# Kernel optimization log

Hardware: AMD Instinct MI355X
Metric: run time of the kernel (lower is better)

Reference implementation:

```python
import jax, jax.numpy as jnp
import numpy as np

B, T = 512, 64
STOCH, DETER, HIDDEN = 30, 200, 200
A, EMBED = 12, 1024
MIN_STD = 0.1
UPDATE_BIAS = -1.0


def _linear_init(key, fan_in, fan_out):
    w_key, b_key = jax.random.split(key)
    lim = 1.0 / np.sqrt(fan_in)
    W = jax.random.uniform(w_key, (fan_in, fan_out), minval=-lim, maxval=lim, dtype=jnp.float32)
    b = jax.random.uniform(b_key, (fan_out,), minval=-lim, maxval=lim, dtype=jnp.float32)
    return W, b


def setup_inputs() -> dict:
    key = jax.random.key(0)
    ks = jax.random.split(key, 12)
    embed = jax.random.normal(ks[0], (B, T, EMBED), dtype=jnp.float32)
    action = jax.random.normal(ks[1], (B, T, A), dtype=jnp.float32)
    noise_prior = jax.random.normal(ks[2], (B, T, STOCH), dtype=jnp.float32)
    noise_post = jax.random.normal(ks[3], (B, T, STOCH), dtype=jnp.float32)
    inp_W, inp_b = _linear_init(ks[4], STOCH + A, HIDDEN)          # _inp_layers
    gru_W, gru_b = _linear_init(ks[5], HIDDEN + DETER, 3 * DETER)  # GRUCell._layer
    img_out_W, img_out_b = _linear_init(ks[6], DETER, HIDDEN)      # _img_out_layers
    ims_W, ims_b = _linear_init(ks[7], HIDDEN, 2 * STOCH)          # _ims_stat_layer
    obs_out_W, obs_out_b = _linear_init(ks[8], DETER + EMBED, HIDDEN)  # _obs_out_layers
    obs_W, obs_b = _linear_init(ks[9], HIDDEN, 2 * STOCH)          # _obs_stat_layer
    return dict(embed=embed, action=action, noise_prior=noise_prior, noise_post=noise_post,
                inp_W=inp_W, inp_b=inp_b, gru_W=gru_W, gru_b=gru_b,
                img_out_W=img_out_W, img_out_b=img_out_b, ims_W=ims_W, ims_b=ims_b,
                obs_out_W=obs_out_W, obs_out_b=obs_out_b, obs_W=obs_W, obs_b=obs_b)


def _observe(embed, action, noise_prior, noise_post,
             inp_W, inp_b, gru_W, gru_b, img_out_W, img_out_b,
             ims_W, ims_b, obs_out_W, obs_out_b, obs_W, obs_b):
    # time-major for scan: [T, B, ...]
    emb_t = jnp.swapaxes(embed, 0, 1)
    act_t = jnp.swapaxes(action, 0, 1)
    npr_t = jnp.swapaxes(noise_prior, 0, 1)
    npo_t = jnp.swapaxes(noise_post, 0, 1)

    def step(carry, xs):
        stoch, deter = carry                    # posterior stoch [B,STOCH], deter [B,DETER]
        a, e, nz_pr, nz_po = xs
        # img_step: input MLP
        x = jax.nn.elu(jnp.concatenate([stoch, a], -1) @ inp_W + inp_b)
        # GRUCell (norm=False)
        parts = jnp.concatenate([x, deter], -1) @ gru_W + gru_b   # [B, 3*DETER]
        reset, cand, update = jnp.split(parts, 3, -1)
        reset = jax.nn.sigmoid(reset)
        cand = jnp.tanh(reset * cand)
        update = jax.nn.sigmoid(update + UPDATE_BIAS)
        deter_new = update * cand + (1.0 - update) * deter
        # prior stats
        h = jax.nn.elu(deter_new @ img_out_W + img_out_b)
        mean_pr, std_pr = jnp.split(h @ ims_W + ims_b, 2, -1)
        std_pr = jax.nn.softplus(std_pr) + MIN_STD
        stoch_pr = mean_pr + std_pr * nz_pr
        # posterior (temp_post=True): cat(deter, embed)
        ho = jax.nn.elu(jnp.concatenate([deter_new, e], -1) @ obs_out_W + obs_out_b)
        mean_po, std_po = jnp.split(ho @ obs_W + obs_b, 2, -1)
        std_po = jax.nn.softplus(std_po) + MIN_STD
        stoch_po = mean_po + std_po * nz_po
        out = (stoch_po, mean_po, std_po, stoch_pr, mean_pr, std_pr, deter_new)
        return (stoch_po, deter_new), out

    init = (jnp.zeros((B, STOCH), jnp.float32), jnp.zeros((B, DETER), jnp.float32))
    _, outs = jax.lax.scan(step, init, (act_t, emb_t, npr_t, npo_t))
    # back to batch-major and pack into a single array [B, T, 6*STOCH + DETER]
    outs = [jnp.swapaxes(o, 0, 1) for o in outs]
    return jnp.concatenate(outs, -1)


def reference(embed, action, noise_prior, noise_post,
              inp_W, inp_b, gru_W, gru_b, img_out_W, img_out_b,
              ims_W, ims_b, obs_out_W, obs_out_b, obs_W, obs_b):
    return _observe(embed, action, noise_prior, noise_post,
                    inp_W, inp_b, gru_W, gru_b, img_out_W, img_out_b,
                    ims_W, ims_b, obs_out_W, obs_out_b, obs_W, obs_b)
```

## Files before the change

### kernel.cpp

```cpp
#include <hip/hip_runtime.h>

typedef _Float16 h2   __attribute__((ext_vector_type(2)));
typedef _Float16 h4   __attribute__((ext_vector_type(4)));
typedef _Float16 half8 __attribute__((ext_vector_type(8)));
typedef float f32x4   __attribute__((ext_vector_type(4)));

#define MFMA16(a,b,c) __builtin_amdgcn_mfma_f32_16x16x32_f16((a),(b),(c),0,0,0)
#define ATOMIC_ST(p,v) __hip_atomic_store((p),(v),__ATOMIC_RELAXED,__HIP_MEMORY_SCOPE_AGENT)
#define ATOMIC_LD(p)   __hip_atomic_load((p),__ATOMIC_RELAXED,__HIP_MEMORY_SCOPE_AGENT)
#define BAR_LDS() do { asm volatile("s_waitcnt lgkmcnt(0)" ::: "memory"); \
                       __builtin_amdgcn_s_barrier();                      \
                       asm volatile("" ::: "memory"); } while (0)


#define EP_HALVES ((size_t)32768*208)

__global__ void prep_frags(const float* __restrict__ inpW, const float* __restrict__ gruW,
                           const float* __restrict__ imgW, const float* __restrict__ obsoutW,
                           const float* __restrict__ imsW, const float* __restrict__ obsW,
                           _Float16* __restrict__ frags) {
    int gb = blockIdx.x, lane = threadIdx.x;
    const float* src; int KS, K, N, ld, roff = 0, local;
    if (gb < 26)       { src = inpW;    KS = 2;  K = 42;   N = 200; ld = 200; local = gb; }
    else if (gb < 520) { src = gruW;    KS = 13; K = 400;  N = 600; ld = 600; local = gb - 26; }
    else if (gb < 611) { src = imgW;    KS = 7;  K = 200;  N = 200; ld = 200; local = gb - 520; }
    else if (gb < 702) { src = obsoutW; KS = 7;  K = 200;  N = 200; ld = 200; local = gb - 611; }
    else if (gb < 730) { src = imsW;    KS = 7;  K = 200;  N = 60;  ld = 60;  local = gb - 702; }
    else if (gb < 758) { src = obsW;    KS = 7;  K = 200;  N = 60;  ld = 60;  local = gb - 730; }
    else               { src = obsoutW; KS = 32; K = 1024; N = 200; ld = 200; roff = 200; local = gb - 758; }
    int nt = local / KS, ks = local % KS;
    int n  = nt * 16 + (lane & 15);
    int k0 = ks * 32 + (lane >> 4) * 8;
    half8 v;
#pragma unroll
    for (int j = 0; j < 8; ++j) {
        int k = k0 + j;
        float f = (k < K && n < N) ? src[(size_t)(k + roff) * ld + n] : 0.0f;
        v[j] = (_Float16)f;
    }
    *(half8*)(frags + (size_t)gb * 512 + lane * 8) = v;
}

__global__ __launch_bounds__(256) void ep_gemm(const float* __restrict__ embed,
                                               const _Float16* __restrict__ w2f,
                                               _Float16* __restrict__ ep) {
    __shared__ __align__(16) _Float16 aE[16 * 1048];
    int tid = threadIdx.x;
    int rb = blockIdx.x * 16;
#pragma unroll
    for (int i = 0; i < 16; ++i) {
        float4 e = *((const float4*)(embed + (size_t)(rb + i) * 1024) + tid);
        h4 hv; hv[0] = (_Float16)e.x; hv[1] = (_Float16)e.y; hv[2] = (_Float16)e.z; hv[3] = (_Float16)e.w;
        *(h4*)(aE + i * 1048 + tid * 4) = hv;
    }
    __syncthreads();
    int w = tid >> 6, lane = tid & 63, m = lane & 15, q = lane >> 4;
    f32x4 acc[4] = {};
    int nts[4]; int ntc = 0;
    for (int nt = w; nt < 13; nt += 4) nts[ntc++] = nt;
    half8 bb[2][4];
#pragma unroll
    for (int j = 0; j < 4; ++j) if (j < ntc)
        bb[0][j] = *(const half8*)(w2f + ((size_t)(nts[j] * 32) * 64 + lane) * 8);
#pragma unroll
    for (int ks = 0; ks < 32; ++ks) {
        int cur = ks & 1, nxt = cur ^ 1;
        if (ks < 31) {
#pragma unroll
            for (int j = 0; j < 4; ++j) if (j < ntc)
                bb[nxt][j] = *(const half8*)(w2f + ((size_t)(nts[j] * 32 + ks + 1) * 64 + lane) * 8);
        }
        half8 a = *(const half8*)(aE + m * 1048 + ks * 32 + q * 8);
#pragma unroll
        for (int j = 0; j < 4; ++j) if (j < ntc)
            acc[j] = MFMA16(a, bb[cur][j], acc[j]);
    }
    for (int j = 0; j < ntc; ++j) {
        int col = nts[j] * 16 + m;
#pragma unroll
        for (int i = 0; i < 4; ++i)
            ep[(size_t)(rb + q * 4 + i) * 208 + col] = (_Float16)acc[j][i];
    }
}

__device__ __forceinline__ float sigm_(float x) { return 1.0f / (1.0f + __expf(-x)); }
__device__ __forceinline__ float tanh_(float x) { float e = __expf(2.0f * x); return 1.0f - 2.0f / (e + 1.0f); }
__device__ __forceinline__ float elu_(float x)  { return x > 0.0f ? x : __expf(x) - 1.0f; }
__device__ __forceinline__ float sp_(float x)   { return fmaxf(x, 0.0f) + log1pf(__expf(-fabsf(x))); }
__device__ __forceinline__ unsigned packh2(float a, float b) {
    h2 p; p[0] = (_Float16)a; p[1] = (_Float16)b;
    return __builtin_bit_cast(unsigned, p);
}

__global__ __launch_bounds__(512) __attribute__((amdgpu_waves_per_eu(2, 2))) void rssm_scan(
    const float* __restrict__ action, const float* __restrict__ npr, const float* __restrict__ npo,
    const float* __restrict__ inp_b, const float* __restrict__ gru_b,
    const float* __restrict__ img_b, const float* __restrict__ obsout_b,
    const float* __restrict__ ims_b, const float* __restrict__ obs_b,
    const _Float16* __restrict__ frags, const _Float16* __restrict__ ep,
    unsigned* __restrict__ qdet, unsigned* __restrict__ stochb,
    unsigned* __restrict__ flags, float* __restrict__ out) {

    __shared__ __align__(16) unsigned actI[16 * 36];
    __shared__ __align__(16) unsigned actG[16 * 212];
    __shared__ __align__(16) unsigned actX[16 * 116];
    __shared__ __align__(16) _Float16 parts[16 * 208];
    __shared__ float statspre[16 * 65];
    __shared__ float bias[1320];

    const _Float16* Finp  = frags;
    const _Float16* Fgru  = frags + (size_t)26  * 512;
    const _Float16* Fimg  = frags + (size_t)520 * 512;
    const _Float16* Fobsd = frags + (size_t)611 * 512;
    const _Float16* Fims  = frags + (size_t)702 * 512;
    const _Float16* Fobs  = frags + (size_t)730 * 512;

    const int tid = threadIdx.x, w = tid >> 6, lane = tid & 63, m = lane & 15, q = lane >> 4;
    const int g = blockIdx.x & 31, wg = blockIdx.x >> 5;
    const int rb = g * 16;
    const bool post = (wg >= 2);
    const bool statside = (wg == 0) || (wg == 2);
    const int colA = w * 16 + m;
    const int colB = (8 + w) * 16 + m;
    unsigned* gf = flags + g * 512;

    for (int i = tid; i < 1320; i += 512) {
        float v;
        if (i < 200) v = inp_b[i];
        else if (i < 800)  v = gru_b[i - 200];
        else if (i < 1000) v = img_b[i - 800];
        else if (i < 1200) v = obsout_b[i - 1000];
        else if (i < 1260) v = ims_b[i - 1200];
        else               v = obs_b[i - 1260];
        bias[i] = v;
    }
    for (int i = tid; i < 16 * 36;  i += 512) actI[i] = 0u;
    for (int i = tid; i < 16 * 212; i += 512) actG[i] = 0u;
    for (int i = tid; i < 16 * 116; i += 512) actX[i] = 0u;

    half8 bgru0[13];
    {
        int tA = (w < 4) ? (3 * wg + w) : (12 + 3 * wg + (w - 4));
#pragma unroll
        for (int ks = 0; ks < 13; ++ks)
            bgru0[ks] = *(const half8*)(Fgru + ((size_t)(tA * 13 + ks) * 64 + lane) * 8);
    }
    half8 bgru1[13];
    if (w < 4) {
        int tB = 25 + 3 * wg + w;
#pragma unroll
        for (int ks = 0; ks < 13; ++ks)
            bgru1[ks] = *(const half8*)(Fgru + ((size_t)(tB * 13 + ks) * 64 + lane) * 8);
    }
    half8 bi0[2], bi1[2];
#pragma unroll
    for (int ks = 0; ks < 2; ++ks)
        bi0[ks] = *(const half8*)(Finp + ((size_t)(w * 2 + ks) * 64 + lane) * 8);
    if (w < 5) {
#pragma unroll
        for (int ks = 0; ks < 2; ++ks)
            bi1[ks] = *(const half8*)(Finp + ((size_t)((8 + w) * 2 + ks) * 64 + lane) * 8);
    }
    const _Float16* F3 = post ? Fobsd : Fimg;
    const _Float16* F4 = post ? Fobs : Fims;
    half8 bp3a[7];
    if (statside) {
#pragma unroll
        for (int ks = 0; ks < 7; ++ks)
            bp3a[ks] = *(const half8*)(F3 + ((size_t)(w * 7 + ks) * 64 + lane) * 8);
    }
    half8 bp4[7];
    if (statside && w >= 4) {
#pragma unroll
        for (int ks = 0; ks < 7; ++ks)
            bp4[ks] = *(const half8*)(F4 + ((size_t)((w - 4) * 7 + ks) * 64 + lane) * 8);
    }
    __syncthreads();

    for (int t = 0; t < 64; ++t) {
        h2 epA[4], epB[4];
        if (post && !(m & 1)) {
#pragma unroll
            for (int i = 0; i < 4; ++i)
                epA[i] = *(const h2*)(ep + ((size_t)(rb + q * 4 + i) * 64 + t) * 208 + colA);
            if (w < 5 && colB < 200) {
#pragma unroll
                for (int i = 0; i < 4; ++i)
                    epB[i] = *(const h2*)(ep + ((size_t)(rb + q * 4 + i) * 64 + t) * 208 + colB);
            }
        }

        if (t > 0 && wg != 2) {
            if (tid == 0) {
                unsigned* f = gf + (t - 1) * 8 + 4;
                int it = 0;
                while (ATOMIC_LD(f) != (unsigned)t) {
                    __builtin_amdgcn_s_sleep(1);
                    if (++it > (1 << 20)) break;
                }
            }
            BAR_LDS();
            __atomic_signal_fence(__ATOMIC_ACQUIRE);
            if (tid < 240) {
                int r = tid / 15, cp = tid % 15;
                actI[r * 36 + cp] =
                    ATOMIC_LD(stochb + (size_t)((((t - 1) & 1) * 32 + g)) * 256 + r * 16 + cp);
            }
        }
        if (tid < 96) {
            int r = tid / 6, cp = tid % 6;
            float2 a2 = *(const float2*)(action + ((size_t)(rb + r) * 64 + t) * 12 + 2 * cp);
            actI[r * 36 + 15 + cp] = packh2(a2.x, a2.y);
        }
        float2 nz = make_float2(0.0f, 0.0f);
        if (statside && tid < 240) {
            int r = tid / 15, cp = tid % 15;
            const float* ns = post ? npo : npr;
            nz = *(const float2*)(ns + ((size_t)(rb + r) * 64 + t) * 30 + 2 * cp);
        }
        BAR_LDS();

        {
            f32x4 acc = {}, acc2 = {};
#pragma unroll
            for (int ks = 0; ks < 2; ++ks) {
                half8 a = *(const half8*)(actI + m * 36 + ks * 16 + q * 4);
                acc = MFMA16(a, bi0[ks], acc);
                if (w < 5) acc2 = MFMA16(a, bi1[ks], acc2);
            }
            f32x4 accN;
#pragma unroll
            for (int i = 0; i < 4; ++i) accN[i] = __shfl_xor(acc[i], 1);
            if (!(m & 1)) {
                int col = w * 16 + m;
#pragma unroll
                for (int i = 0; i < 4; ++i)
                    actG[(q * 4 + i) * 212 + (col >> 1)] =
                        packh2(elu_(acc[i] + bias[col]), elu_(accN[i] + bias[col + 1]));
            }
            if (w < 5) {
                f32x4 acc2N;
#pragma unroll
                for (int i = 0; i < 4; ++i) acc2N[i] = __shfl_xor(acc2[i], 1);
                if (!(m & 1)) {
                    int col = (8 + w) * 16 + m;
                    if (col < 200) {
#pragma unroll
                        for (int i = 0; i < 4; ++i)
                            actG[(q * 4 + i) * 212 + (col >> 1)] =
                                packh2(elu_(acc2[i] + bias[col]), elu_(acc2N[i] + bias[col + 1]));
                    }
                }
            }
        }
        BAR_LDS();

        {
            f32x4 a0 = {}, a1 = {};
#pragma unroll
            for (int ks = 0; ks < 13; ++ks) {
                half8 a = *(const half8*)(actG + m * 212 + ks * 16 + q * 4);
                a0 = MFMA16(a, bgru0[ks], a0);
                if (w < 4) a1 = MFMA16(a, bgru1[ks], a1);
            }
#pragma unroll
            for (int i = 0; i < 4; ++i)
                parts[(q * 4 + i) * 208 + w * 16 + m] = (_Float16)a0[i];
            if (w < 4) {
#pragma unroll
                for (int i = 0; i < 4; ++i)
                    parts[(q * 4 + i) * 208 + (8 + w) * 16 + m] = (_Float16)a1[i];
            }
        }
        half8 pf3[7];
        if (statside && w < 5) {
#pragma unroll
            for (int ks = 0; ks < 7; ++ks)
                pf3[ks] = *(const half8*)(F3 + ((size_t)((8 + w) * 7 + ks) * 64 + lane) * 8);
        }
        BAR_LDS();

        unsigned* qd = qdet + (size_t)((t & 1) * 32 + g) * 1600;
        float gdn0 = 0.0f, gdn1 = 0.0f; int gr = 0, gn0 = 0;
        if (tid < 400) {
            int r = tid / 25, p = tid % 25;
            int n0 = 50 * wg + 2 * p;
            float pg[3][2];
#pragma unroll
            for (int j = 0; j < 3; ++j) {
                int cg = n0 + 200 * j;
                int bj = (j == 0) ? 3 * wg : (j == 1) ? 12 + 3 * wg : 25 + 3 * wg;
                int lt = 4 * j + (cg >> 4) - bj;
                h2 v = *(const h2*)(parts + r * 208 + lt * 16 + (cg & 15));
                pg[j][0] = (float)v[0] + bias[200 + cg];
                pg[j][1] = (float)v[1] + bias[200 + cg + 1];
            }
            h2 dold = *(const h2*)&actG[r * 212 + 100 + (n0 >> 1)];
            float dn[2];
#pragma unroll
            for (int e = 0; e < 2; ++e) {
                float reset = sigm_(pg[0][e]);
                float cand  = tanh_(reset * pg[1][e]);
                float upd   = sigm_(pg[2][e] - 1.0f);
                dn[e] = upd * cand + (1.0f - upd) * (float)dold[e];
            }
            unsigned pk = packh2(dn[0], dn[1]);
            actG[r * 212 + 100 + (n0 >> 1)] = pk;
            ATOMIC_ST(qd + r * 100 + (n0 >> 1), pk);
            gdn0 = dn[0]; gdn1 = dn[1]; gr = r; gn0 = n0;
        }
        __syncthreads();

        __atomic_signal_fence(__ATOMIC_RELEASE);
        if (tid == 0) ATOMIC_ST(gf + t * 8 + wg, (unsigned)(t + 1));
        if (tid < 400)
            *(float2*)(out + ((size_t)(rb + gr) * 64 + t) * 380 + 180 + gn0) = make_float2(gdn0, gdn1);
        if (tid < 3) {
            unsigned* f = gf + t * 8 + ((wg + 1 + tid) & 3);
            int it = 0;
            while (ATOMIC_LD(f) != (unsigned)(t + 1)) {
                __builtin_amdgcn_s_sleep(1);
                if (++it > (1 << 20)) break;
            }
        }
        BAR_LDS();
        __atomic_signal_fence(__ATOMIC_ACQUIRE);
        for (int i = tid; i < 1200; i += 512) {
            int r = i / 75, idx = i % 75;
            int pp = (25 * (wg + 1) + idx) % 100;
            actG[r * 212 + 100 + pp] = ATOMIC_LD(qd + r * 100 + pp);
        }
        BAR_LDS();

        if (statside) {
            f32x4 acc = {}, acc2 = {};
#pragma unroll
            for (int ks = 0; ks < 7; ++ks) {
                half8 a = *(const half8*)(actG + m * 212 + 100 + ks * 16 + q * 4);
                acc = MFMA16(a, bp3a[ks], acc);
                if (w < 5) acc2 = MFMA16(a, pf3[ks], acc2);
            }
            f32x4 accN;
#pragma unroll
            for (int i = 0; i < 4; ++i) accN[i] = __shfl_xor(acc[i], 1);
            if (!(m & 1)) {
                int bb0 = post ? 1000 : 800;
#pragma unroll
                for (int i = 0; i < 4; ++i) {
                    float e0 = post ? (float)epA[i][0] : 0.0f;
                    float e1 = post ? (float)epA[i][1] : 0.0f;
                    actX[(q * 4 + i) * 116 + (colA >> 1)] =
                        packh2(elu_(acc[i] + bias[bb0 + colA] + e0),
                               elu_(accN[i] + bias[bb0 + colA + 1] + e1));
                }
            }
            if (w < 5) {
                f32x4 acc2N;
#pragma unroll
                for (int i = 0; i < 4; ++i) acc2N[i] = __shfl_xor(acc2[i], 1);
                if (!(m & 1) && colB < 200) {
                    int bb0 = post ? 1000 : 800;
#pragma unroll
                    for (int i = 0; i < 4; ++i) {
                        float e0 = post ? (float)epB[i][0] : 0.0f;
                        float e1 = post ? (float)epB[i][1] : 0.0f;
                        actX[(q * 4 + i) * 116 + (colB >> 1)] =
                            packh2(elu_(acc2[i] + bias[bb0 + colB] + e0),
                                   elu_(acc2N[i] + bias[bb0 + colB + 1] + e1));
                    }
                }
            }
        }
        BAR_LDS();

        if (statside && w >= 4) {
            f32x4 acc = {};
#pragma unroll
            for (int ks = 0; ks < 7; ++ks) {
                half8 a = *(const half8*)(actX + m * 116 + ks * 16 + q * 4);
                acc = MFMA16(a, bp4[ks], acc);
            }
#pragma unroll
            for (int i = 0; i < 4; ++i)
                statspre[(q * 4 + i) * 65 + (w - 4) * 16 + m] = acc[i];
        }
        BAR_LDS();

        float o0v = 0.f, o1v = 0.f, o2v = 0.f, o3v = 0.f, o4v = 0.f, o5v = 0.f;
        int pr = 0, pcp = 0; bool doout = false;
        if (statside && tid < 240) {
            int r = tid / 15, cp = tid % 15;
            int bb0 = post ? 1260 : 1200;
            float m0 = statspre[r * 65 + 2 * cp]     + bias[bb0 + 2 * cp];
            float m1 = statspre[r * 65 + 2 * cp + 1] + bias[bb0 + 2 * cp + 1];
            float s0 = sp_(statspre[r * 65 + 30 + 2 * cp]     + bias[bb0 + 30 + 2 * cp]) + 0.1f;
            float s1 = sp_(statspre[r * 65 + 30 + 2 * cp + 1] + bias[bb0 + 30 + 2 * cp + 1]) + 0.1f;
            float st0 = m0 + s0 * nz.x, st1 = m1 + s1 * nz.y;
            if (post) {
                unsigned pk = packh2(st0, st1);
                actI[r * 36 + cp] = pk;
                ATOMIC_ST(stochb + (size_t)((t & 1) * 32 + g) * 256 + r * 16 + cp, pk);
            }
            o0v = st0; o1v = st1; o2v = m0; o3v = m1; o4v = s0; o5v = s1;
            pr = r; pcp = cp; doout = true;
        }
        __syncthreads();
        if (wg == 2 && t < 63) {
            __atomic_signal_fence(__ATOMIC_RELEASE);
            if (tid == 0) ATOMIC_ST(gf + t * 8 + 4, (unsigned)(t + 1));
        }
        if (doout) {
            size_t ob = ((size_t)(rb + pr) * 64 + t) * 380;
            int o0 = post ? 0 : 90;
            *(float2*)(out + ob + o0 + 2 * pcp)      = make_float2(o0v, o1v);
            *(float2*)(out + ob + o0 + 30 + 2 * pcp) = make_float2(o2v, o3v);
            *(float2*)(out + ob + o0 + 60 + 2 * pcp) = make_float2(o4v, o5v);
        }
    }
}

extern "C" void kernel_launch(void* const* d_in, const int* in_sizes, int n_in,
                              void* d_out, int out_size, void* d_ws, size_t ws_size,
                              hipStream_t stream) {
    const float* embed   = (const float*)d_in[0];
    const float* action  = (const float*)d_in[1];
    const float* npr     = (const float*)d_in[2];
    const float* npo     = (const float*)d_in[3];
    const float* inpW    = (const float*)d_in[4];
    const float* inpb    = (const float*)d_in[5];
    const float* gruW    = (const float*)d_in[6];
    const float* grub    = (const float*)d_in[7];
    const float* imgW    = (const float*)d_in[8];
    const float* imgb    = (const float*)d_in[9];
    const float* imsW    = (const float*)d_in[10];
    const float* imsb    = (const float*)d_in[11];
    const float* obsoutW = (const float*)d_in[12];
    const float* obsoutb = (const float*)d_in[13];
    const float* obsW    = (const float*)d_in[14];
    const float* obsb    = (const float*)d_in[15];

    char* ws = (char*)d_ws;
    _Float16* ep     = (_Float16*)ws;
    _Float16* frags  = (_Float16*)(ws + EP_HALVES * 2);
    char* p          = ws + EP_HALVES * 2 + (size_t)1174 * 1024;
    unsigned* qdetb  = (unsigned*)p;
    p += (size_t)2 * 32 * 1600 * 4;
    unsigned* stochb = (unsigned*)p;
    p += (size_t)2 * 32 * 256 * 4;
    unsigned* flags  = (unsigned*)p;

    prep_frags<<<1174, 64, 0, stream>>>(inpW, gruW, imgW, obsoutW, imsW, obsW, frags);
    ep_gemm<<<2048, 256, 0, stream>>>(embed, frags + (size_t)758 * 512, ep);
    rssm_scan<<<128, 512, 0, stream>>>(action, npr, npo, inpb, grub, imgb, obsoutb,
                                       imsb, obsb, frags, ep, qdetb, stochb, flags,
                                       (float*)d_out);
}
```

Measured before the change: 948.8 us.

## Replace flag-based cross-block sync with tagged 64-bit data words polled per element

Cross-workgroup exchange of the deter and stoch state now packs a step tag into the upper half of each 64-bit word. Consumers poll each word until its tag matches, which removes the separate flag stores, the flag polling and several block-wide barriers on each timestep. The ep intermediate is also stored with a row stride of 200 instead of 208, and ep_gemm zeroes the exchange buffers so stale tags from earlier runs cannot match. The cost is wider atomics, more polling traffic from many threads, and a reliance on ordering between each 64-bit store and its payload.

```diff
diff --git a/kernel.cpp b/kernel.cpp
--- a/kernel.cpp
+++ b/kernel.cpp
@@ -4,16 +4,18 @@
 typedef _Float16 h4   __attribute__((ext_vector_type(4)));
 typedef _Float16 half8 __attribute__((ext_vector_type(8)));
 typedef float f32x4   __attribute__((ext_vector_type(4)));
+typedef unsigned long long u64;
 
 #define MFMA16(a,b,c) __builtin_amdgcn_mfma_f32_16x16x32_f16((a),(b),(c),0,0,0)
-#define ATOMIC_ST(p,v) __hip_atomic_store((p),(v),__ATOMIC_RELAXED,__HIP_MEMORY_SCOPE_AGENT)
-#define ATOMIC_LD(p)   __hip_atomic_load((p),__ATOMIC_RELAXED,__HIP_MEMORY_SCOPE_AGENT)
+#define ATOMIC_ST64(p,v) __hip_atomic_store((p),(v),__ATOMIC_RELAXED,__HIP_MEMORY_SCOPE_AGENT)
+#define ATOMIC_LD64(p)   __hip_atomic_load((p),__ATOMIC_RELAXED,__HIP_MEMORY_SCOPE_AGENT)
 #define BAR_LDS() do { asm volatile("s_waitcnt lgkmcnt(0)" ::: "memory"); \
                        __builtin_amdgcn_s_barrier();                      \
                        asm volatile("" ::: "memory"); } while (0)
 
 
-#define EP_HALVES ((size_t)32768*208)
+#define EP_HALVES ((size_t)32768*200)
+#define ZWORDS 118784
 
 __global__ void prep_frags(const float* __restrict__ inpW, const float* __restrict__ gruW,
                            const float* __restrict__ imgW, const float* __restrict__ obsoutW,
@@ -43,7 +45,12 @@
 
 __global__ __launch_bounds__(256) void ep_gemm(const float* __restrict__ embed,
                                                const _Float16* __restrict__ w2f,
-                                               _Float16* __restrict__ ep) {
+                                               _Float16* __restrict__ ep,
+                                               u64* __restrict__ zmem) {
+    {
+        int gid = blockIdx.x * 256 + threadIdx.x;
+        if (gid < ZWORDS) zmem[gid] = 0ull;
+    }
     __shared__ __align__(16) _Float16 aE[16 * 1048];
     int tid = threadIdx.x;
     int rb = blockIdx.x * 16;
@@ -77,9 +84,11 @@
     }
     for (int j = 0; j < ntc; ++j) {
         int col = nts[j] * 16 + m;
-#pragma unroll
-        for (int i = 0; i < 4; ++i)
-            ep[(size_t)(rb + q * 4 + i) * 208 + col] = (_Float16)acc[j][i];
+        if (col < 200) {
+#pragma unroll
+            for (int i = 0; i < 4; ++i)
+                ep[(size_t)(rb + q * 4 + i) * 200 + col] = (_Float16)acc[j][i];
+        }
     }
 }
 
@@ -91,6 +100,15 @@
     h2 p; p[0] = (_Float16)a; p[1] = (_Float16)b;
     return __builtin_bit_cast(unsigned, p);
 }
+__device__ __forceinline__ unsigned poll64(const u64* p, unsigned want, u64 v) {
+    int it = 0;
+    while ((unsigned)(v >> 32) != want) {
+        __builtin_amdgcn_s_sleep(1);
+        v = ATOMIC_LD64(p);
+        if (++it > (1 << 20)) break;
+    }
+    return (unsigned)v;
+}
 
 __global__ __launch_bounds__(512) __attribute__((amdgpu_waves_per_eu(2, 2))) void rssm_scan(
     const float* __restrict__ action, const float* __restrict__ npr, const float* __restrict__ npo,
@@ -98,8 +116,8 @@
     const float* __restrict__ img_b, const float* __restrict__ obsout_b,
     const float* __restrict__ ims_b, const float* __restrict__ obs_b,
     const _Float16* __restrict__ frags, const _Float16* __restrict__ ep,
-    unsigned* __restrict__ qdet, unsigned* __restrict__ stochb,
-    unsigned* __restrict__ flags, float* __restrict__ out) {
+    u64* __restrict__ qdet, u64* __restrict__ stochb,
+    float* __restrict__ out) {
 
     __shared__ __align__(16) unsigned actI[16 * 36];
     __shared__ __align__(16) unsigned actG[16 * 212];
@@ -122,7 +140,6 @@
     const bool statside = (wg == 0) || (wg == 2);
     const int colA = w * 16 + m;
     const int colB = (8 + w) * 16 + m;
-    unsigned* gf = flags + g * 512;
 
     for (int i = tid; i < 1320; i += 512) {
         float v;
@@ -182,35 +199,17 @@
         if (post && !(m & 1)) {
 #pragma unroll
             for (int i = 0; i < 4; ++i)
-                epA[i] = *(const h2*)(ep + ((size_t)(rb + q * 4 + i) * 64 + t) * 208 + colA);
+                epA[i] = *(const h2*)(ep + ((size_t)(rb + q * 4 + i) * 64 + t) * 200 + colA);
             if (w < 5 && colB < 200) {
 #pragma unroll
                 for (int i = 0; i < 4; ++i)
-                    epB[i] = *(const h2*)(ep + ((size_t)(rb + q * 4 + i) * 64 + t) * 208 + colB);
-            }
-        }
-
-        if (t > 0 && wg != 2) {
-            if (tid == 0) {
-                unsigned* f = gf + (t - 1) * 8 + 4;
-                int it = 0;
-                while (ATOMIC_LD(f) != (unsigned)t) {
-                    __builtin_amdgcn_s_sleep(1);
-                    if (++it > (1 << 20)) break;
-                }
-            }
-            BAR_LDS();
-            __atomic_signal_fence(__ATOMIC_ACQUIRE);
-            if (tid < 240) {
-                int r = tid / 15, cp = tid % 15;
-                actI[r * 36 + cp] =
-                    ATOMIC_LD(stochb + (size_t)((((t - 1) & 1) * 32 + g)) * 256 + r * 16 + cp);
-            }
-        }
+                    epB[i] = *(const h2*)(ep + ((size_t)(rb + q * 4 + i) * 64 + t) * 200 + colB);
+            }
+        }
+        float2 a2 = make_float2(0.0f, 0.0f);
         if (tid < 96) {
             int r = tid / 6, cp = tid % 6;
-            float2 a2 = *(const float2*)(action + ((size_t)(rb + r) * 64 + t) * 12 + 2 * cp);
-            actI[r * 36 + 15 + cp] = packh2(a2.x, a2.y);
+            a2 = *(const float2*)(action + ((size_t)(rb + r) * 64 + t) * 12 + 2 * cp);
         }
         float2 nz = make_float2(0.0f, 0.0f);
         if (statside && tid < 240) {
@@ -218,6 +217,16 @@
             const float* ns = post ? npo : npr;
             nz = *(const float2*)(ns + ((size_t)(rb + r) * 64 + t) * 30 + 2 * cp);
         }
+
+        if (t > 0 && wg != 2 && tid < 240) {
+            int r = tid / 15, cp = tid % 15;
+            const u64* sp = stochb + (size_t)(((t - 1) & 1) * 32 + g) * 256 + r * 16 + cp;
+            actI[r * 36 + cp] = poll64(sp, (unsigned)t, ATOMIC_LD64(sp));
+        }
+        if (tid < 96) {
+            int r = tid / 6, cp = tid % 6;
+            actI[r * 36 + 15 + cp] = packh2(a2.x, a2.y);
+        }
         BAR_LDS();
 
         {
@@ -280,8 +289,7 @@
         }
         BAR_LDS();
 
-        unsigned* qd = qdet + (size_t)((t & 1) * 32 + g) * 1600;
-        float gdn0 = 0.0f, gdn1 = 0.0f; int gr = 0, gn0 = 0;
+        u64* qd = qdet + (size_t)((t & 1) * 32 + g) * 1600;
         if (tid < 400) {
             int r = tid / 25, p = tid % 25;
             int n0 = 50 * wg + 2 * p;
@@ -305,30 +313,25 @@
                 dn[e] = upd * cand + (1.0f - upd) * (float)dold[e];
             }
             unsigned pk = packh2(dn[0], dn[1]);
+            ATOMIC_ST64(qd + r * 100 + (n0 >> 1), ((u64)(unsigned)(t + 1) << 32) | pk);
             actG[r * 212 + 100 + (n0 >> 1)] = pk;
-            ATOMIC_ST(qd + r * 100 + (n0 >> 1), pk);
-            gdn0 = dn[0]; gdn1 = dn[1]; gr = r; gn0 = n0;
-        }
-        __syncthreads();
-
-        __atomic_signal_fence(__ATOMIC_RELEASE);
-        if (tid == 0) ATOMIC_ST(gf + t * 8 + wg, (unsigned)(t + 1));
-        if (tid < 400)
-            *(float2*)(out + ((size_t)(rb + gr) * 64 + t) * 380 + 180 + gn0) = make_float2(gdn0, gdn1);
-        if (tid < 3) {
-            unsigned* f = gf + t * 8 + ((wg + 1 + tid) & 3);
-            int it = 0;
-            while (ATOMIC_LD(f) != (unsigned)(t + 1)) {
-                __builtin_amdgcn_s_sleep(1);
-                if (++it > (1 << 20)) break;
-            }
-        }
-        BAR_LDS();
-        __atomic_signal_fence(__ATOMIC_ACQUIRE);
-        for (int i = tid; i < 1200; i += 512) {
-            int r = i / 75, idx = i % 75;
-            int pp = (25 * (wg + 1) + idx) % 100;
-            actG[r * 212 + 100 + pp] = ATOMIC_LD(qd + r * 100 + pp);
+            *(float2*)(out + ((size_t)(rb + r) * 64 + t) * 380 + 180 + n0) = make_float2(dn[0], dn[1]);
+        }
+
+        {
+            unsigned want = (unsigned)(t + 1);
+            int i0 = tid, i1 = tid + 512, i2 = tid + 1024;
+            int r0 = i0 / 75, p0 = (25 * (wg + 1) + i0 % 75) % 100;
+            int r1 = i1 / 75, p1 = (25 * (wg + 1) + i1 % 75) % 100;
+            int r2 = 0, p2 = 0;
+            bool h2ok = i2 < 1200;
+            if (h2ok) { r2 = i2 / 75; p2 = (25 * (wg + 1) + i2 % 75) % 100; }
+            u64 v0 = ATOMIC_LD64(qd + r0 * 100 + p0);
+            u64 v1 = ATOMIC_LD64(qd + r1 * 100 + p1);
+            u64 v2 = h2ok ? ATOMIC_LD64(qd + r2 * 100 + p2) : 0ull;
+            actG[r0 * 212 + 100 + p0] = poll64(qd + r0 * 100 + p0, want, v0);
+            actG[r1 * 212 + 100 + p1] = poll64(qd + r1 * 100 + p1, want, v1);
+            if (h2ok) actG[r2 * 212 + 100 + p2] = poll64(qd + r2 * 100 + p2, want, v2);
         }
         BAR_LDS();
 
@@ -386,8 +389,6 @@
         }
         BAR_LDS();
 
-        float o0v = 0.f, o1v = 0.f, o2v = 0.f, o3v = 0.f, o4v = 0.f, o5v = 0.f;
-        int pr = 0, pcp = 0; bool doout = false;
         if (statside && tid < 240) {
             int r = tid / 15, cp = tid % 15;
             int bb0 = post ? 1260 : 1200;
@@ -398,23 +399,15 @@
             float st0 = m0 + s0 * nz.x, st1 = m1 + s1 * nz.y;
             if (post) {
                 unsigned pk = packh2(st0, st1);
+                ATOMIC_ST64(stochb + (size_t)((t & 1) * 32 + g) * 256 + r * 16 + cp,
+                            ((u64)(unsigned)(t + 1) << 32) | pk);
                 actI[r * 36 + cp] = pk;
-                ATOMIC_ST(stochb + (size_t)((t & 1) * 32 + g) * 256 + r * 16 + cp, pk);
-            }
-            o0v = st0; o1v = st1; o2v = m0; o3v = m1; o4v = s0; o5v = s1;
-            pr = r; pcp = cp; doout = true;
-        }
-        __syncthreads();
-        if (wg == 2 && t < 63) {
-            __atomic_signal_fence(__ATOMIC_RELEASE);
-            if (tid == 0) ATOMIC_ST(gf + t * 8 + 4, (unsigned)(t + 1));
-        }
-        if (doout) {
-            size_t ob = ((size_t)(rb + pr) * 64 + t) * 380;
+            }
+            size_t ob = ((size_t)(rb + r) * 64 + t) * 380;
             int o0 = post ? 0 : 90;
-            *(float2*)(out + ob + o0 + 2 * pcp)      = make_float2(o0v, o1v);
-            *(float2*)(out + ob + o0 + 30 + 2 * pcp) = make_float2(o2v, o3v);
-            *(float2*)(out + ob + o0 + 60 + 2 * pcp) = make_float2(o4v, o5v);
+            *(float2*)(out + ob + o0 + 2 * cp)      = make_float2(st0, st1);
+            *(float2*)(out + ob + o0 + 30 + 2 * cp) = make_float2(m0, m1);
+            *(float2*)(out + ob + o0 + 60 + 2 * cp) = make_float2(s0, s1);
         }
     }
 }
@@ -443,15 +436,13 @@
     _Float16* ep     = (_Float16*)ws;
     _Float16* frags  = (_Float16*)(ws + EP_HALVES * 2);
     char* p          = ws + EP_HALVES * 2 + (size_t)1174 * 1024;
-    unsigned* qdetb  = (unsigned*)p;
-    p += (size_t)2 * 32 * 1600 * 4;
-    unsigned* stochb = (unsigned*)p;
-    p += (size_t)2 * 32 * 256 * 4;
-    unsigned* flags  = (unsigned*)p;
+    u64* qdetb       = (u64*)p;
+    p += (size_t)2 * 32 * 1600 * 8;
+    u64* stochb      = (u64*)p;
 
     prep_frags<<<1174, 64, 0, stream>>>(inpW, gruW, imgW, obsoutW, imsW, obsW, frags);
-    ep_gemm<<<2048, 256, 0, stream>>>(embed, frags + (size_t)758 * 512, ep);
+    ep_gemm<<<2048, 256, 0, stream>>>(embed, frags + (size_t)758 * 512, ep, qdetb);
     rssm_scan<<<128, 512, 0, stream>>>(action, npr, npo, inpb, grub, imgb, obsoutb,
-                                       imsb, obsb, frags, ep, qdetb, stochb, flags,
+                                       imsb, obsb, frags, ep, qdetb, stochb,
                                        (float*)d_out);
 }
```

Measured after the change: 1.010 ms. 1.06x slower.
